# Kernel optimization log

Measured on AMD Instinct MI355X. Metric: run time of the kernel, lower is better.

## Reference

```python
import jax, jax.numpy as jnp
import numpy as np

B, T, C, E = 8, 8192, 256, 64
CAPACITY_FACTOR = 1.25
TOP_K = 2


def setup_inputs() -> dict:
    key = jax.random.key(0)
    k1, k2, k3 = jax.random.split(key, 3)
    x = jax.random.normal(k1, (B, T, C), dtype=jnp.float32)
    W_gate = jax.random.normal(k2, (C, E), dtype=jnp.float32) / np.sqrt(C)
    W_experts = jax.random.normal(k3, (E, C, C), dtype=jnp.float32) / np.sqrt(C)
    return {"x": x, "W_gate": W_gate, "W_experts": W_experts}


def reference(x, W_gate, W_experts):
    b, t, c = x.shape
    e = W_gate.shape[1]
    n = b * t              # tokens
    s = n * TOP_K          # assignment slots, ordered (token i, slot j) like the torch loop
    capacity = max(1, int(CAPACITY_FACTOR * s / e))  # static python int

    logits = x @ W_gate                              # [B,T,E]
    gates = jax.nn.softmax(logits, axis=-1)
    scores, indices = jax.lax.top_k(gates, TOP_K)    # [B,T,2] (values are raw gate probs, no renorm)

    x_flat = x.reshape(n, c)
    eid = indices.reshape(s)                         # expert id per assignment, FIFO order i*2+j
    sc = scores.reshape(s)
    tok = jnp.repeat(jnp.arange(n), TOP_K)           # source token per assignment

    # FIFO rank of each assignment within its expert (matches the python capacity loop)
    onehot = jax.nn.one_hot(eid, e, dtype=jnp.int32)          # [S,E]
    rank = jnp.cumsum(onehot, axis=0)[jnp.arange(s), eid] - 1  # prior count of same expert
    keep = rank < capacity                                     # capacity-dropped tokens

    # Scatter tokens into per-expert buffers [E*capacity, C]; dropped slots go OOB -> 'drop'
    buf_idx = jnp.where(keep, eid * capacity + rank, e * capacity)
    buf = jnp.zeros((e * capacity, c), x.dtype).at[buf_idx].set(x_flat[tok], mode="drop")

    # Grouped GEMM: one Linear(C,C) per expert
    y = jnp.einsum("eck,ekd->ecd", buf.reshape(e, capacity, c), W_experts)
    y = y.reshape(e * capacity, c)

    # Gather back, scale by gate score, scatter-add into token positions
    safe_idx = jnp.where(keep, buf_idx, 0)
    contrib = jnp.where(keep[:, None], y[safe_idx] * sc[:, None], jnp.zeros((), x.dtype))
    combined = jnp.zeros((n, c), x.dtype).at[tok].add(contrib).reshape(b, t, c)

    load = gates.mean(axis=(0, 1))                  # [E]
    aux_loss = jnp.mean((load - 1.0 / e) ** 2)      # mse vs uniform
    return combined, aux_loss
```

## Files before the change

kernel.cpp:

```cpp
#include <hip/hip_runtime.h>
#include <stdint.h>

#define N_TOK   65536
#define S_SLOTS 131072
#define NEXP    64
#define CDIM    256
#define CAP     2560
#define NCHUNK  1024

typedef unsigned short u16;
typedef float    fvec4  __attribute__((ext_vector_type(4)));
typedef float    f32x4  __attribute__((ext_vector_type(4)));
typedef __bf16   bf16x8 __attribute__((ext_vector_type(8)));
typedef unsigned short u16x4 __attribute__((ext_vector_type(4)));

typedef __attribute__((address_space(1))) const void gvoid_t;
typedef __attribute__((address_space(3))) void       svoid_t;

__device__ __forceinline__ u16 f2bf(float f) {
  uint32_t u = __builtin_bit_cast(uint32_t, f);
  u += 0x7fffu + ((u >> 16) & 1u);
  return (u16)(u >> 16);
}
__device__ __forceinline__ float bf2f(u16 h) {
  return __builtin_bit_cast(float, (uint32_t)h << 16);
}
__device__ __forceinline__ void gload16(const void* g, void* l) {
  __builtin_amdgcn_global_load_lds(
      reinterpret_cast<gvoid_t*>(reinterpret_cast<uintptr_t>(g)),
      reinterpret_cast<svoid_t*>(reinterpret_cast<uintptr_t>(l)),
      16, 0, 0);
}

__global__ __launch_bounds__(256) void gating_kernel(
    const float* __restrict__ x, const float* __restrict__ Wg,
    u16* __restrict__ x_bf16, float* __restrict__ slot_score,
    int* __restrict__ slot_eid, float* __restrict__ load_g,
    int* __restrict__ chunk_hist)
{
  __shared__ float smem[8448];
  __shared__ int   hist_s[64];
  float* W_s   = smem;
  float* A_s   = smem + 4096;
  float* L_s   = smem;
  float* PMAXs = smem + 4160;
  float* PV1   = smem + 4416;
  int*   PI1   = (int*)(smem + 4672);
  float* PV2   = smem + 4928;
  int*   PI2   = (int*)(smem + 5184);
  float* PSUM  = smem + 5440;
  float* RINVs = smem + 5696;
  float* PLOAD = smem + 5760;

  const int t  = threadIdx.x;
  const int m0 = blockIdx.x * 64;
  const int ty = t >> 4, tx = t & 15;

  if (t < 64) hist_s[t] = 0;

  float acc[4][4];
#pragma unroll
  for (int j = 0; j < 4; ++j)
#pragma unroll
    for (int i = 0; i < 4; ++i) acc[j][i] = 0.f;

  for (int kt = 0; kt < 4; ++kt) {
    const int k0 = kt * 64;
#pragma unroll
    for (int p = 0; p < 4; ++p) {
      int idx = p * 1024 + t * 4;
      int kk = idx >> 6, e = idx & 63;
      *(fvec4*)&W_s[kk * 64 + e] = *(const fvec4*)&Wg[(size_t)(k0 + kk) * 64 + e];
    }
#pragma unroll
    for (int p = 0; p < 4; ++p) {
      int idx = p * 1024 + t * 4;
      int m = idx >> 6, k = idx & 63;
      fvec4 v = *(const fvec4*)&x[(size_t)(m0 + m) * 256 + k0 + k];
      *(fvec4*)&A_s[m * 68 + k] = v;
      u16x4 h;
      h.x = f2bf(v.x); h.y = f2bf(v.y); h.z = f2bf(v.z); h.w = f2bf(v.w);
      *(u16x4*)&x_bf16[(size_t)(m0 + m) * 256 + k0 + k] = h;
    }
    __syncthreads();
#pragma unroll
    for (int k4 = 0; k4 < 16; ++k4) {
      fvec4 av[4], bv[4];
#pragma unroll
      for (int j = 0; j < 4; ++j)
        av[j] = *(const fvec4*)&A_s[(ty * 4 + j) * 68 + k4 * 4];
#pragma unroll
      for (int kk = 0; kk < 4; ++kk)
        bv[kk] = *(const fvec4*)&W_s[(k4 * 4 + kk) * 64 + tx * 4];
#pragma unroll
      for (int j = 0; j < 4; ++j)
#pragma unroll
        for (int i = 0; i < 4; ++i) {
          acc[j][i] = fmaf(av[j][0], bv[0][i], acc[j][i]);
          acc[j][i] = fmaf(av[j][1], bv[1][i], acc[j][i]);
          acc[j][i] = fmaf(av[j][2], bv[2][i], acc[j][i]);
          acc[j][i] = fmaf(av[j][3], bv[3][i], acc[j][i]);
        }
    }
    __syncthreads();
  }

#pragma unroll
  for (int j = 0; j < 4; ++j)
#pragma unroll
    for (int i = 0; i < 4; ++i)
      L_s[(ty * 4 + j) * 65 + tx * 4 + i] = acc[j][i];
  __syncthreads();

  const int w = t >> 6, lane = t & 63;

  float pm = -3.4e38f, a1 = -3.4e38f, a2 = -3.4e38f;
  int   j1 = 0, j2 = 0;
#pragma unroll
  for (int ii = 0; ii < 16; ++ii) {
    int e = w * 16 + ii;
    float lg = L_s[lane * 65 + e];
    pm = fmaxf(pm, lg);
    if (lg > a1)      { a2 = a1; j2 = j1; a1 = lg; j1 = e; }
    else if (lg > a2) { a2 = lg; j2 = e; }
  }
  PMAXs[w * 64 + lane] = pm;
  PV1[w * 64 + lane] = a1; PI1[w * 64 + lane] = j1;
  PV2[w * 64 + lane] = a2; PI2[w * 64 + lane] = j2;
  __syncthreads();

  float m  = PMAXs[lane];
  float v1 = PV1[lane]; int i1 = PI1[lane];
  float v2 = PV2[lane]; int i2 = PI2[lane];
#pragma unroll
  for (int ww = 1; ww < 4; ++ww) {
    m = fmaxf(m, PMAXs[ww * 64 + lane]);
    float b1 = PV1[ww * 64 + lane]; int bi1 = PI1[ww * 64 + lane];
    float b2 = PV2[ww * 64 + lane]; int bi2 = PI2[ww * 64 + lane];
    if (b1 > v1) {
      if (v1 >= b2) { v2 = v1; i2 = i1; } else { v2 = b2; i2 = bi2; }
      v1 = b1; i1 = bi1;
    } else if (b1 > v2) { v2 = b1; i2 = bi1; }
  }

  float s = 0.f;
#pragma unroll
  for (int ii = 0; ii < 16; ++ii) {
    int e = w * 16 + ii;
    float E = __expf(L_s[lane * 65 + e] - m);
    L_s[lane * 65 + e] = E;
    s += E;
  }
  PSUM[w * 64 + lane] = s;
  __syncthreads();

  if (w == 0) {
    float rs = PSUM[lane] + PSUM[64 + lane] + PSUM[128 + lane] + PSUM[192 + lane];
    float ri = 1.0f / rs;
    RINVs[lane] = ri;
    float sc1 = L_s[lane * 65 + i1] * ri;
    float sc2 = L_s[lane * 65 + i2] * ri;
    int tg = m0 + lane;
    slot_eid[2 * tg]     = i1;
    slot_eid[2 * tg + 1] = i2;
    slot_score[2 * tg]     = sc1;
    slot_score[2 * tg + 1] = sc2;
    atomicAdd(&hist_s[i1], 1);
    atomicAdd(&hist_s[i2], 1);
  }
  __syncthreads();

  {
    float sl = 0.f;
#pragma unroll
    for (int jj = 0; jj < 16; ++jj) {
      int j = w * 16 + jj;
      sl = fmaf(L_s[j * 65 + lane], RINVs[j], sl);
    }
    PLOAD[t] = sl;
  }
  __syncthreads();
  if (t < 64) {
    float sl = PLOAD[t] + PLOAD[64 + t] + PLOAD[128 + t] + PLOAD[192 + t];
    atomicAdd(&load_g[t], sl);
    chunk_hist[blockIdx.x * 64 + t] = hist_s[t];
  }
}

__global__ __launch_bounds__(256) void wtrans_kernel(
    const float* __restrict__ W, u16* __restrict__ WT)
{
  __shared__ float tile[64 * 65];
  const int b = blockIdx.x;
  const int e = b >> 4, tt = b & 15;
  const int k0 = (tt >> 2) * 64, d0 = (tt & 3) * 64;
  const int t = threadIdx.x;
  const int j = t & 63, i0 = t >> 6;
  const float* We = W + (size_t)e * 65536;
#pragma unroll
  for (int p = 0; p < 16; ++p) {
    int i = p * 4 + i0;
    tile[i * 65 + j] = We[(size_t)(k0 + i) * 256 + d0 + j];
  }
  __syncthreads();
  u16* WTe = WT + (size_t)e * 65536;
#pragma unroll
  for (int p = 0; p < 16; ++p) {
    int d = p * 4 + i0;
    WTe[(size_t)(d0 + d) * 256 + k0 + j] = f2bf(tile[j * 65 + d]);
  }
}

__global__ __launch_bounds__(256) void scan_kernel(int* __restrict__ hist,
                                                   int* __restrict__ tot)
{
  const int e = blockIdx.x;
  const int t = threadIdx.x;
  const int lane = t & 63, w = t >> 6;
  int h[4];
#pragma unroll
  for (int i = 0; i < 4; ++i) h[i] = hist[(t * 4 + i) * 64 + e];
  int local = h[0] + h[1] + h[2] + h[3];
  int v = local;
#pragma unroll
  for (int off = 1; off < 64; off <<= 1) {
    int u = __shfl_up(v, off);
    if (lane >= off) v += u;
  }
  __shared__ int wtot[4];
  if (lane == 63) wtot[w] = v;
  __syncthreads();
  int woff = 0;
  for (int i = 0; i < w; ++i) woff += wtot[i];
  int excl = woff + v - local;
  if (t == 255) tot[e] = woff + v;
  hist[(t * 4 + 0) * 64 + e] = excl;
  hist[(t * 4 + 1) * 64 + e] = excl + h[0];
  hist[(t * 4 + 2) * 64 + e] = excl + h[0] + h[1];
  hist[(t * 4 + 3) * 64 + e] = excl + h[0] + h[1] + h[2];
}

__global__ __launch_bounds__(128) void rank_kernel(
    const int* __restrict__ slot_eid, const int* __restrict__ base,
    int* __restrict__ slot2buf, int* __restrict__ row_token)
{
  const int c = blockIdx.x;
  const int t = threadIdx.x;
  const int s = c * 128 + t;
  const int lane = t & 63, w = t >> 6;
  const int e = slot_eid[s];
  __shared__ int hist0[64];
  if (t < 64) hist0[t] = 0;
  __syncthreads();
  int rank = 0, cnt = 0;
#pragma unroll
  for (int k = 0; k < 64; ++k) {
    int eo = __shfl(e, k);
    bool m = (eo == e);
    rank += (m && k < lane) ? 1 : 0;
    cnt  += m ? 1 : 0;
  }
  if (w == 0 && rank == cnt - 1) hist0[e] = cnt;
  __syncthreads();
  int g = base[c * 64 + e] + rank + (w ? hist0[e] : 0);
  if (g < CAP) {
    slot2buf[s] = e * CAP + g;
    row_token[e * CAP + g] = s >> 1;
  } else {
    slot2buf[s] = -1;
  }
}

__global__ __launch_bounds__(256) void gemm_kernel(
    const u16* __restrict__ x_bf16, const u16* __restrict__ WT,
    const int* __restrict__ row_token, const int* __restrict__ tot,
    u16* __restrict__ y)
{
  __shared__ u16 A_s[128 * 64];
  __shared__ u16 B_s[128 * 64];
  __shared__ int tok_s[128];

  const int b = blockIdx.x;
  const int e = b / 40;
  const int r = b % 40;
  const int m0 = (r >> 1) * 128, n0 = (r & 1) * 128;
  const int t = threadIdx.x;

  if (m0 >= tot[e]) return;

  if (t < 128) tok_s[t] = row_token[e * CAP + m0 + t];
  __syncthreads();

  const int w = t >> 6, lane = t & 63;
  const int rsub8 = lane >> 3;
  const int c8    = lane & 7;
  const int csw   = (c8 ^ rsub8) * 8;

  const u16* WTe = WT + (size_t)e * 65536;

  const int wm = w & 1, wn = w >> 1;
  const int lr = lane & 15, q = lane >> 4;

  f32x4 acc[4][4];
#pragma unroll
  for (int mt = 0; mt < 4; ++mt)
#pragma unroll
    for (int nt = 0; nt < 4; ++nt) acc[mt][nt] = (f32x4){0.f, 0.f, 0.f, 0.f};

  for (int kt = 0; kt < 4; ++kt) {
    const int k0 = kt * 64;
#pragma unroll
    for (int i = 0; i < 4; ++i) {
      int ra = w * 32 + i * 8 + rsub8;
      gload16(x_bf16 + (size_t)tok_s[ra] * 256 + k0 + csw,
              (char*)A_s + (size_t)(w * 32 + i * 8) * 128);
      gload16(WTe + (size_t)(n0 + ra) * 256 + k0 + csw,
              (char*)B_s + (size_t)(w * 32 + i * 8) * 128);
    }
    __syncthreads();
#pragma unroll
    for (int kk = 0; kk < 2; ++kk) {
      bf16x8 af[4], bg[4];
#pragma unroll
      for (int mt = 0; mt < 4; ++mt) {
        int row = wm * 64 + mt * 16 + lr;
        af[mt] = *(const bf16x8*)&A_s[row * 64 + (((kk * 4 + q) ^ (lr & 7)) * 8)];
      }
#pragma unroll
      for (int nt = 0; nt < 4; ++nt) {
        int row = wn * 64 + nt * 16 + lr;
        bg[nt] = *(const bf16x8*)&B_s[row * 64 + (((kk * 4 + q) ^ (lr & 7)) * 8)];
      }
#pragma unroll
      for (int mt = 0; mt < 4; ++mt)
#pragma unroll
        for (int nt = 0; nt < 4; ++nt)
          acc[mt][nt] = __builtin_amdgcn_mfma_f32_16x16x32_bf16(
              af[mt], bg[nt], acc[mt][nt], 0, 0, 0);
    }
    __syncthreads();
  }

  u16* ye = y + (size_t)e * CAP * 256;
#pragma unroll
  for (int mt = 0; mt < 4; ++mt) {
    int grow = m0 + wm * 64 + mt * 16 + q * 4;
#pragma unroll
    for (int nt = 0; nt < 4; ++nt) {
      int gcol = n0 + wn * 64 + nt * 16 + lr;
#pragma unroll
      for (int rr = 0; rr < 4; ++rr)
        ye[(size_t)(grow + rr) * 256 + gcol] = f2bf(acc[mt][nt][rr]);
    }
  }
}

__global__ __launch_bounds__(256) void combine_kernel(
    const u16* __restrict__ y, const int* __restrict__ slot2buf,
    const float* __restrict__ slot_score, float* __restrict__ out)
{
  const int tok  = blockIdx.x * 4 + (threadIdx.x >> 6);
  const int lane = threadIdx.x & 63;
  const int   p0 = slot2buf[2 * tok],   p1 = slot2buf[2 * tok + 1];
  const float s0 = slot_score[2 * tok], s1 = slot_score[2 * tok + 1];
  float o0 = 0.f, o1 = 0.f, o2 = 0.f, o3 = 0.f;
  if (p0 >= 0) {
    u16x4 h = *(const u16x4*)&y[(size_t)p0 * 256 + lane * 4];
    o0 = fmaf(s0, bf2f(h.x), o0); o1 = fmaf(s0, bf2f(h.y), o1);
    o2 = fmaf(s0, bf2f(h.z), o2); o3 = fmaf(s0, bf2f(h.w), o3);
  }
  if (p1 >= 0) {
    u16x4 h = *(const u16x4*)&y[(size_t)p1 * 256 + lane * 4];
    o0 = fmaf(s1, bf2f(h.x), o0); o1 = fmaf(s1, bf2f(h.y), o1);
    o2 = fmaf(s1, bf2f(h.z), o2); o3 = fmaf(s1, bf2f(h.w), o3);
  }
  fvec4 o = {o0, o1, o2, o3};
  *(fvec4*)&out[(size_t)tok * 256 + lane * 4] = o;
}

__global__ __launch_bounds__(64) void aux_kernel(
    const float* __restrict__ load_g, float* __restrict__ out_aux)
{
  const int lane = threadIdx.x;
  float l = load_g[lane] * (1.0f / 65536.0f) - (1.0f / 64.0f);
  float v = l * l;
#pragma unroll
  for (int off = 1; off < 64; off <<= 1) v += __shfl_xor(v, off);
  if (lane == 0) out_aux[0] = v * (1.0f / 64.0f);
}

extern "C" void kernel_launch(void* const* d_in, const int* in_sizes, int n_in,
                              void* d_out, int out_size, void* d_ws, size_t ws_size,
                              hipStream_t stream)
{
  const float* x  = (const float*)d_in[0];
  const float* Wg = (const float*)d_in[1];
  const float* We = (const float*)d_in[2];
  float* out = (float*)d_out;

  char* ws = (char*)d_ws;
  float* slot_score = (float*)(ws + 0);
  int*   slot_eid   = (int*)(ws + 524288);
  int*   slot2buf   = (int*)(ws + 1048576);
  int*   row_token  = (int*)(ws + 1572864);
  float* load_g     = (float*)(ws + 2228224);
  int*   chunk_hist = (int*)(ws + 2359296);
  int*   tot        = (int*)(ws + 2621440);
  u16*   x_bf16     = (u16*)(ws + 4194304);
  u16*   WT         = (u16*)(ws + 37748736);
  u16*   y          = (u16*)(ws + 46137344);

  hipMemsetAsync(row_token, 0, 655360, stream);
  hipMemsetAsync(load_g, 0, 256, stream);

  gating_kernel<<<1024, 256, 0, stream>>>(x, Wg, x_bf16, slot_score, slot_eid,
                                          load_g, chunk_hist);
  wtrans_kernel<<<1024, 256, 0, stream>>>(We, WT);
  scan_kernel<<<64, 256, 0, stream>>>(chunk_hist, tot);
  rank_kernel<<<1024, 128, 0, stream>>>(slot_eid, chunk_hist, slot2buf, row_token);
  gemm_kernel<<<2560, 256, 0, stream>>>(x_bf16, WT, row_token, tot, y);
  combine_kernel<<<16384, 256, 0, stream>>>(y, slot2buf, slot_score, out);
  aux_kernel<<<1, 64, 0, stream>>>(load_g, out + 16777216);
}
```

Before: 231.2 us.

## Merge gating with weight transpose, fold aux into combine, drop row_token memset

Interleaves the weight-transpose blocks with the gating blocks in one launch, so the bandwidth-bound transpose overlaps the gating compute and one launch disappears. The aux-loss reduction moves into block 0 of the combine kernel, and the row_token memset is replaced by bounds-guarded token loads in the GEMM. The GEMM block index is also remapped so that concurrently scheduled blocks spread across experts. Risks: the merged kernel's register and shared-memory footprint is set by the larger gating path, and the remap changes cache locality of the expert weights.

```diff
diff --git a/kernel.cpp b/kernel.cpp
--- a/kernel.cpp
+++ b/kernel.cpp
@@ -32,14 +32,41 @@
       16, 0, 0);
 }
 
-__global__ __launch_bounds__(256) void gating_kernel(
+__global__ __launch_bounds__(256) void gating_wtrans_kernel(
     const float* __restrict__ x, const float* __restrict__ Wg,
-    u16* __restrict__ x_bf16, float* __restrict__ slot_score,
-    int* __restrict__ slot_eid, float* __restrict__ load_g,
-    int* __restrict__ chunk_hist)
+    const float* __restrict__ We_g, u16* __restrict__ x_bf16,
+    float* __restrict__ slot_score, int* __restrict__ slot_eid,
+    float* __restrict__ load_g, int* __restrict__ chunk_hist,
+    u16* __restrict__ WT)
 {
   __shared__ float smem[8448];
   __shared__ int   hist_s[64];
+
+  const int blk = blockIdx.x;
+
+  if (blk & 1) {
+    float* tile = smem;
+    const int b = blk >> 1;
+    const int e = b >> 4, tt = b & 15;
+    const int k0 = (tt >> 2) * 64, d0 = (tt & 3) * 64;
+    const int t = threadIdx.x;
+    const int j = t & 63, i0 = t >> 6;
+    const float* We = We_g + (size_t)e * 65536;
+#pragma unroll
+    for (int p = 0; p < 16; ++p) {
+      int i = p * 4 + i0;
+      tile[i * 65 + j] = We[(size_t)(k0 + i) * 256 + d0 + j];
+    }
+    __syncthreads();
+    u16* WTe = WT + (size_t)e * 65536;
+#pragma unroll
+    for (int p = 0; p < 16; ++p) {
+      int d = p * 4 + i0;
+      WTe[(size_t)(d0 + d) * 256 + k0 + j] = f2bf(tile[j * 65 + d]);
+    }
+    return;
+  }
+
   float* W_s   = smem;
   float* A_s   = smem + 4096;
   float* L_s   = smem;
@@ -52,8 +79,9 @@
   float* RINVs = smem + 5696;
   float* PLOAD = smem + 5760;
 
+  const int cid = blk >> 1;
   const int t  = threadIdx.x;
-  const int m0 = blockIdx.x * 64;
+  const int m0 = cid * 64;
   const int ty = t >> 4, tx = t & 15;
 
   if (t < 64) hist_s[t] = 0;
@@ -183,31 +211,7 @@
   if (t < 64) {
     float sl = PLOAD[t] + PLOAD[64 + t] + PLOAD[128 + t] + PLOAD[192 + t];
     atomicAdd(&load_g[t], sl);
-    chunk_hist[blockIdx.x * 64 + t] = hist_s[t];
-  }
-}
-
-__global__ __launch_bounds__(256) void wtrans_kernel(
-    const float* __restrict__ W, u16* __restrict__ WT)
-{
-  __shared__ float tile[64 * 65];
-  const int b = blockIdx.x;
-  const int e = b >> 4, tt = b & 15;
-  const int k0 = (tt >> 2) * 64, d0 = (tt & 3) * 64;
-  const int t = threadIdx.x;
-  const int j = t & 63, i0 = t >> 6;
-  const float* We = W + (size_t)e * 65536;
-#pragma unroll
-  for (int p = 0; p < 16; ++p) {
-    int i = p * 4 + i0;
-    tile[i * 65 + j] = We[(size_t)(k0 + i) * 256 + d0 + j];
-  }
-  __syncthreads();
-  u16* WTe = WT + (size_t)e * 65536;
-#pragma unroll
-  for (int p = 0; p < 16; ++p) {
-    int d = p * 4 + i0;
-    WTe[(size_t)(d0 + d) * 256 + k0 + j] = f2bf(tile[j * 65 + d]);
+    chunk_hist[cid * 64 + t] = hist_s[t];
   }
 }
 
@@ -280,15 +284,18 @@
   __shared__ u16 B_s[128 * 64];
   __shared__ int tok_s[128];
 
-  const int b = blockIdx.x;
+  const int bl = blockIdx.x;
+  const int b = (bl & 7) * 320 + (bl >> 3);
   const int e = b / 40;
   const int r = b % 40;
   const int m0 = (r >> 1) * 128, n0 = (r & 1) * 128;
   const int t = threadIdx.x;
 
-  if (m0 >= tot[e]) return;
-
-  if (t < 128) tok_s[t] = row_token[e * CAP + m0 + t];
+  const int te = tot[e];
+  if (m0 >= te) return;
+
+  if (t < 128)
+    tok_s[t] = (m0 + t < te) ? row_token[e * CAP + m0 + t] : 0;
   __syncthreads();
 
   const int w = t >> 6, lane = t & 63;
@@ -357,8 +364,17 @@
 
 __global__ __launch_bounds__(256) void combine_kernel(
     const u16* __restrict__ y, const int* __restrict__ slot2buf,
-    const float* __restrict__ slot_score, float* __restrict__ out)
-{
+    const float* __restrict__ slot_score, float* __restrict__ out,
+    const float* __restrict__ load_g, float* __restrict__ out_aux)
+{
+  if (blockIdx.x == 0 && threadIdx.x < 64) {
+    const int lane = threadIdx.x;
+    float l = load_g[lane] * (1.0f / 65536.0f) - (1.0f / 64.0f);
+    float v = l * l;
+#pragma unroll
+    for (int off = 1; off < 64; off <<= 1) v += __shfl_xor(v, off);
+    if (lane == 0) out_aux[0] = v * (1.0f / 64.0f);
+  }
   const int tok  = blockIdx.x * 4 + (threadIdx.x >> 6);
   const int lane = threadIdx.x & 63;
   const int   p0 = slot2buf[2 * tok],   p1 = slot2buf[2 * tok + 1];
@@ -376,17 +392,6 @@
   }
   fvec4 o = {o0, o1, o2, o3};
   *(fvec4*)&out[(size_t)tok * 256 + lane * 4] = o;
-}
-
-__global__ __launch_bounds__(64) void aux_kernel(
-    const float* __restrict__ load_g, float* __restrict__ out_aux)
-{
-  const int lane = threadIdx.x;
-  float l = load_g[lane] * (1.0f / 65536.0f) - (1.0f / 64.0f);
-  float v = l * l;
-#pragma unroll
-  for (int off = 1; off < 64; off <<= 1) v += __shfl_xor(v, off);
-  if (lane == 0) out_aux[0] = v * (1.0f / 64.0f);
 }
 
 extern "C" void kernel_launch(void* const* d_in, const int* in_sizes, int n_in,
@@ -410,15 +415,13 @@
   u16*   WT         = (u16*)(ws + 37748736);
   u16*   y          = (u16*)(ws + 46137344);
 
-  hipMemsetAsync(row_token, 0, 655360, stream);
   hipMemsetAsync(load_g, 0, 256, stream);
 
-  gating_kernel<<<1024, 256, 0, stream>>>(x, Wg, x_bf16, slot_score, slot_eid,
-                                          load_g, chunk_hist);
-  wtrans_kernel<<<1024, 256, 0, stream>>>(We, WT);
+  gating_wtrans_kernel<<<2048, 256, 0, stream>>>(x, Wg, We, x_bf16, slot_score,
+                                                 slot_eid, load_g, chunk_hist, WT);
   scan_kernel<<<64, 256, 0, stream>>>(chunk_hist, tot);
   rank_kernel<<<1024, 128, 0, stream>>>(slot_eid, chunk_hist, slot2buf, row_token);
   gemm_kernel<<<2560, 256, 0, stream>>>(x_bf16, WT, row_token, tot, y);
-  combine_kernel<<<16384, 256, 0, stream>>>(y, slot2buf, slot_score, out);
-  aux_kernel<<<1, 64, 0, stream>>>(load_g, out + 16777216);
-}
+  combine_kernel<<<16384, 256, 0, stream>>>(y, slot2buf, slot_score, out,
+                                            load_g, out + 16777216);
+}
```

Result: slower. 242.9 us (+5.0%).
